# Performance work log

Hardware: AMD Instinct MI355X
Metric: run time of the kernel (lower is better)

The kernel has to match this reference:

```python
import jax, jax.numpy as jnp
import numpy as np

M_HIST = 5        # Anderson history depth (m=5 in anderson_solver)
N_POWER = 20      # power iterations to estimate sigma for spectral_norm
REG = 1e-4        # Tikhonov regularization on the Anderson LS system
MAX_ITER = 25     # deq_max_iter


def _l2norm(x):
    return x / (jnp.linalg.norm(x) + 1e-12)


def spectral_normalize(W):
    # torch spectral_norm: W / sigma, sigma = u^T W v with u,v from power iteration
    u = _l2norm(jnp.ones((W.shape[0],), W.dtype))
    def body(_, u):
        v = _l2norm(W.T @ u)
        return _l2norm(W @ v)
    u = jax.lax.fori_loop(0, N_POWER, body, u)
    v = _l2norm(W.T @ u)
    u = jax.lax.stop_gradient(u)
    v = jax.lax.stop_gradient(v)
    sigma = u @ (W @ v)
    return W / sigma


def make_f(W1, b1, W2, b2):
    W1s = spectral_normalize(W1)
    W2s = spectral_normalize(W2)
    def f(z, context):
        h = jnp.tanh(jnp.concatenate([z, context], axis=-1) @ W1s.T + b1)
        return jnp.tanh(h @ W2s.T + b2)
    return f


def anderson(f, x0, context, max_iter, m=M_HIST):
    # Mirrors anderson_solver, including its duplicated warm-up step.
    X = [x0]
    F = [f(x0, context)]
    x = F[0]; X.append(x); F.append(f(x, context))
    x = F[0]; X.append(x); F.append(f(x, context))
    for _k in range(2, max_iter):
        m_k = min(len(X) - 1, m)
        dX = jnp.stack([X[-i] - X[-i - 1] for i in range(1, m_k + 1)], axis=-1)  # [B,d,mk]
        dF = jnp.stack([F[-i] - F[-i - 1] for i in range(1, m_k + 1)], axis=-1)
        dG = dF - dX
        A = jnp.einsum('bdi,bdj->bij', dG, dG) + REG * jnp.eye(m_k, dtype=x0.dtype)
        r = F[-1] - X[-1]
        Bv = jnp.einsum('bdi,bd->bi', dG, r)
        alpha = jnp.linalg.solve(A, Bv[..., None])[..., 0]          # [B,mk]
        x = F[-1] - jnp.einsum('bdi,bi->bd', dF, alpha)
        X.append(x)
        F.append(f(x, context))
        if len(X) > m + 1:
            X.pop(0); F.pop(0)
    return X[-1]


def setup_inputs() -> dict:
    key = jax.random.key(0)
    ks = jax.random.split(key, 5)
    B, X_DIM, LATENT, HIDDEN = 2048, 256, 256, 1024
    context = jax.random.normal(ks[0], (B, X_DIM), jnp.float32)
    W1 = jax.random.normal(ks[1], (HIDDEN, LATENT + X_DIM), jnp.float32) / np.sqrt(LATENT + X_DIM)
    b1 = jax.random.normal(ks[2], (HIDDEN,), jnp.float32) * 0.01
    W2 = jax.random.normal(ks[3], (LATENT, HIDDEN), jnp.float32) / np.sqrt(HIDDEN)
    b2 = jax.random.normal(ks[4], (LATENT,), jnp.float32) * 0.01
    return {"context": context, "W1": W1, "b1": b1, "W2": W2, "b2": b2}


def reference(context, W1, b1, W2, b2):
    f = make_f(W1, b1, W2, b2)
    z0 = jnp.zeros((context.shape[0], W2.shape[0]), context.dtype)
    z_star = anderson(f, z0, context, MAX_ITER)
    return z_star
```

## Files before the change

kernel.cpp:

```cpp
#include <hip/hip_runtime.h>
#include <hip/hip_bf16.h>


#define B_ROWS 2048
#define D_LAT  256
#define D_CTX  256
#define D_HID  1024
#define KCAT   512
#define SLOT   (B_ROWS * D_LAT)
#define NRING  7

typedef __bf16 bf16x8 __attribute__((ext_vector_type(8)));
typedef float f32x4 __attribute__((ext_vector_type(4)));
typedef unsigned short u16;

__global__ void init_kernel(const float* __restrict__ ctx,
                            __hip_bfloat16* __restrict__ zc,
                            float* __restrict__ vA, float* __restrict__ uA,
                            float* __restrict__ G1p, float* __restrict__ G2) {
  int i = blockIdx.x * 256 + threadIdx.x;
  if (i < B_ROWS * KCAT) {
    int b = i >> 9, c = i & 511;
    float v = (c < 256) ? 0.0f : ctx[b * 256 + (c - 256)];
    zc[i] = __float2bfloat16(v);
  }
  if (i < 512 * 512) G1p[i] = 0.0f;
  if (i < 256 * 256) G2[i] = 0.0f;
  if (i < KCAT) vA[i] = 0.0f;
  if (i < D_LAT) uA[i] = 1.0f;
}

__global__ __launch_bounds__(256) void gram_kernel(
    const float* __restrict__ W1, const float* __restrict__ W2,
    float* __restrict__ G1p, float* __restrict__ G2) {
  __shared__ float As[32][66];
  __shared__ float Bs[32][34];
  const int tid = threadIdx.x;
  const int tx = tid & 15, ty = tid >> 4;

  const float* X; float* G; int N, ti, tj, k0base; bool modeA;
  int b = blockIdx.x;
  if (b < 1024) {
    modeA = true; X = W1; G = G1p; N = 512;
    int s = b >> 7, t = b & 127;
    ti = t >> 4; tj = t & 15; k0base = s * 128;
  } else {
    modeA = false; b -= 1024; X = W2; G = G2; N = 256;
    int s = b >> 5, t = b & 31;
    ti = t >> 3; tj = t & 7; k0base = s * 128;
  }

  float acc[4][2] = {};
  for (int k0 = k0base; k0 < k0base + 128; k0 += 32) {
    if (modeA) {
      for (int idx = tid; idx < 2048; idx += 256) {
        int r = idx & 63, c = idx >> 6;
        As[c][r] = X[(size_t)(k0 + c) * 512 + ti * 64 + r];
      }
      for (int idx = tid; idx < 1024; idx += 256) {
        int r = idx & 31, c = idx >> 5;
        Bs[c][r] = X[(size_t)(k0 + c) * 512 + tj * 32 + r];
      }
    } else {
      for (int idx = tid; idx < 2048; idx += 256) {
        int c = idx & 31, r = idx >> 5;
        As[c][r] = X[(size_t)(ti * 64 + r) * 1024 + k0 + c];
      }
      for (int idx = tid; idx < 1024; idx += 256) {
        int c = idx & 31, r = idx >> 5;
        Bs[c][r] = X[(size_t)(tj * 32 + r) * 1024 + k0 + c];
      }
    }
    __syncthreads();
#pragma unroll
    for (int kk = 0; kk < 32; kk++) {
      const float2* ap = (const float2*)&As[kk][ty * 4];
      float2 a0 = ap[0], a1 = ap[1];
      float2 b0 = *(const float2*)&Bs[kk][tx * 2];
      float a[4] = {a0.x, a0.y, a1.x, a1.y};
      float bb[2] = {b0.x, b0.y};
#pragma unroll
      for (int i = 0; i < 4; i++)
#pragma unroll
        for (int j = 0; j < 2; j++) acc[i][j] += a[i] * bb[j];
    }
    __syncthreads();
  }
#pragma unroll
  for (int i = 0; i < 4; i++)
#pragma unroll
    for (int j = 0; j < 2; j++)
      atomicAdd(&G[(size_t)(ti * 64 + ty * 4 + i) * N + tj * 32 + tx * 2 + j],
                acc[i][j]);
}

__global__ __launch_bounds__(256) void colsum_kernel(
    const float* __restrict__ W1, float* __restrict__ vA) {
  int b = blockIdx.x;
  for (int c = threadIdx.x; c < KCAT; c += 256) {
    float s = 0.f;
#pragma unroll
    for (int r = 0; r < 16; r++) s += W1[(size_t)(16 * b + r) * KCAT + c];
    atomicAdd(&vA[c], s);
  }
}

__global__ __launch_bounds__(256) void pmv_kernel(
    const float* __restrict__ G1p, const float* __restrict__ G2,
    const float* __restrict__ vi, float* __restrict__ vo,
    const float* __restrict__ ui, float* __restrict__ uo, int g1_active) {
  int gw = blockIdx.x * 4 + (threadIdx.x >> 6);
  int lane = threadIdx.x & 63;
  const float* G; const float* in; float* out; int n, r;
  if (gw < 512) {
    if (!g1_active) return;
    G = G1p; in = vi; out = vo; n = 512; r = gw;
  } else {
    G = G2; in = ui; out = uo; n = 256; r = gw - 512;
  }
  const float4* Gr = (const float4*)(G + (size_t)r * n);
  const float4* uv = (const float4*)in;
  float acc = 0.f;
  for (int c = lane; c < (n >> 2); c += 64) {
    float4 g = Gr[c], u = uv[c];
    acc += g.x * u.x + g.y * u.y + g.z * u.z + g.w * u.w;
  }
  for (int off = 32; off; off >>= 1) acc += __shfl_down(acc, off, 64);
  if (lane == 0) out[r] = 0.25f * acc;
}

__global__ __launch_bounds__(256) void sigma_kernel(
    const float* __restrict__ vA, const float* __restrict__ vB,
    const float* __restrict__ uA, const float* __restrict__ uB,
    float* __restrict__ sig) {
  float s[4] = {0.f, 0.f, 0.f, 0.f};
  for (int i = threadIdx.x; i < KCAT; i += 256) {
    s[0] += vA[i] * vB[i];
    s[1] += vA[i] * vA[i];
  }
  for (int i = threadIdx.x; i < D_LAT; i += 256) {
    s[2] += uA[i] * uA[i];
    s[3] += uA[i] * uB[i];
  }
  __shared__ float red[4][4];
  int lane = threadIdx.x & 63, w = threadIdx.x >> 6;
  for (int k = 0; k < 4; k++) {
    float a = s[k];
    for (int off = 32; off; off >>= 1) a += __shfl_down(a, off, 64);
    if (lane == 0) red[k][w] = a;
  }
  __syncthreads();
  if (threadIdx.x == 0) {
    float d0 = red[0][0] + red[0][1] + red[0][2] + red[0][3];
    float d1 = red[1][0] + red[1][1] + red[1][2] + red[1][3];
    float d2 = red[2][0] + red[2][1] + red[2][2] + red[2][3];
    float d3 = red[3][0] + red[3][1] + red[3][2] + red[3][3];
    sig[0] = sqrtf(0.25f * d0 / d1);
    sig[1] = sqrtf(0.25f * d2 / d3);
  }
}

__global__ void wfold_kernel(const float* __restrict__ W1,
                             const float* __restrict__ W2,
                             const float* __restrict__ sig,
                             __hip_bfloat16* __restrict__ W1b,
                             __hip_bfloat16* __restrict__ W2b) {
  int i = blockIdx.x * 256 + threadIdx.x;
  if (i < D_HID * KCAT) W1b[i] = __float2bfloat16(W1[i] * sig[0]);
  int j = i - D_HID * KCAT;
  if (j >= 0 && j < D_LAT * D_HID) W2b[j] = __float2bfloat16(W2[j] * sig[1]);
}

__global__ void warm1_kernel(const float* __restrict__ Fh,
                             float* __restrict__ Xh,
                             __hip_bfloat16* __restrict__ zc) {
  int i = blockIdx.x * 256 + threadIdx.x;
  float v = Fh[i];
  Xh[SLOT + i] = v;
  zc[(i >> 8) * KCAT + (i & 255)] = __float2bfloat16(v);
}
__global__ void warm2_kernel(const float* __restrict__ Fh,
                             float* __restrict__ Xh, float* __restrict__ Fw) {
  int i = blockIdx.x * 256 + threadIdx.x;
  Xh[2 * SLOT + i] = Fh[i];
  Fw[2 * SLOT + i] = Fh[SLOT + i];
}

template <int BM, int BN, bool OUT_BF16>
__global__ __launch_bounds__(256) void gemm_mfma(
    const __hip_bfloat16* __restrict__ A, const __hip_bfloat16* __restrict__ W,
    int K, const float* __restrict__ bias, float* __restrict__ Cf,
    __hip_bfloat16* __restrict__ Cb, int N) {
  __shared__ __align__(16) u16 lds[(BM + BN) * 64];
  u16* As = lds;
  u16* Ws = lds + BM * 64;
  const int tid = threadIdx.x;
  const int lane = tid & 63;
  const int wid = tid >> 6;
  const int wy = wid >> 1, wx = wid & 1;
  constexpr int WM = BM / 2, WN = BN / 2;
  constexpr int MB = WM / 16, NB = WN / 16;
  const int bm = blockIdx.x * BM;
  const int bn = blockIdx.y * BN;
  const int rlo = lane & 15, quad = lane >> 4;

  f32x4 acc[MB][NB] = {};

  for (int k0 = 0; k0 < K; k0 += 64) {
    for (int c = tid; c < BM * 8; c += 256) {
      int r = c >> 3, o = (c & 7) ^ (r & 7);
      __builtin_amdgcn_global_load_lds(
          (const __attribute__((address_space(1))) void*)(A + (size_t)(bm + r) * K + k0 + o * 8),
          (__attribute__((address_space(3))) void*)(As + c * 8), 16, 0, 0);
    }
    for (int c = tid; c < BN * 8; c += 256) {
      int r = c >> 3, o = (c & 7) ^ (r & 7);
      __builtin_amdgcn_global_load_lds(
          (const __attribute__((address_space(1))) void*)(W + (size_t)(bn + r) * K + k0 + o * 8),
          (__attribute__((address_space(3))) void*)(Ws + c * 8), 16, 0, 0);
    }
    __syncthreads();
#pragma unroll
    for (int kk = 0; kk < 2; kk++) {
      bf16x8 af[MB], bfr[NB];
#pragma unroll
      for (int mb = 0; mb < MB; mb++) {
        int r = wy * WM + mb * 16 + rlo;
        int o = (kk * 4 + quad) ^ (r & 7);
        af[mb] = *(const bf16x8*)(As + (r * 8 + o) * 8);
      }
#pragma unroll
      for (int nb = 0; nb < NB; nb++) {
        int r = wx * WN + nb * 16 + rlo;
        int o = (kk * 4 + quad) ^ (r & 7);
        bfr[nb] = *(const bf16x8*)(Ws + (r * 8 + o) * 8);
      }
#pragma unroll
      for (int mb = 0; mb < MB; mb++)
#pragma unroll
        for (int nb = 0; nb < NB; nb++)
          acc[mb][nb] = __builtin_amdgcn_mfma_f32_16x16x32_bf16(
              af[mb], bfr[nb], acc[mb][nb], 0, 0, 0);
    }
    __syncthreads();
  }

#pragma unroll
  for (int mb = 0; mb < MB; mb++) {
#pragma unroll
    for (int nb = 0; nb < NB; nb++) {
      int n = bn + wx * WN + nb * 16 + rlo;
      float bv = bias[n];
#pragma unroll
      for (int rg = 0; rg < 4; rg++) {
        int m = bm + wy * WM + mb * 16 + quad * 4 + rg;
        float val = tanhf(acc[mb][nb][rg] + bv);
        if constexpr (OUT_BF16) {
          Cb[(size_t)m * N + n] = __float2bfloat16(val);
        } else {
          Cf[(size_t)m * N + n] = val;
        }
      }
    }
  }
}

template <int MK>
__global__ __launch_bounds__(256) void anderson_step_kernel(
    const float* __restrict__ Xh, const float* __restrict__ Fh,
    float* __restrict__ Xw, __hip_bfloat16* __restrict__ zc, int t) {
  const int lane = threadIdx.x & 63;
  const int wid = threadIdx.x >> 6;
  const int b = blockIdx.x * 4 + wid;
  const int base = b * D_LAT + 4 * lane;

  f32x4 f[MK + 1], x[MK + 1];
#pragma unroll
  for (int i = 0; i <= MK; i++) {
    int sl = (t - 1 - i) % NRING;
    f[i] = *(const f32x4*)(Fh + (size_t)sl * SLOT + base);
    x[i] = *(const f32x4*)(Xh + (size_t)sl * SLOT + base);
  }

  const f32x4 r = f[0] - x[0];
  f32x4 dF[MK], dG[MK];
#pragma unroll
  for (int i = 0; i < MK; i++) {
    dF[i] = f[i] - f[i + 1];
    dG[i] = dF[i] - (x[i] - x[i + 1]);
  }

  constexpr int NV = MK * (MK + 1) / 2 + MK;
  float vals[NV];
  {
    int p = 0;
#pragma unroll
    for (int i = 0; i < MK; i++)
#pragma unroll
      for (int j = i; j < MK; j++) {
        f32x4 q = dG[i] * dG[j];
        vals[p++] = q[0] + q[1] + q[2] + q[3];
      }
#pragma unroll
    for (int i = 0; i < MK; i++) {
      f32x4 q = dG[i] * r;
      vals[p++] = q[0] + q[1] + q[2] + q[3];
    }
  }
#pragma unroll
  for (int off = 1; off <= 32; off <<= 1)
#pragma unroll
    for (int v = 0; v < NV; v++) vals[v] += __shfl_xor(vals[v], off, 64);

  float A[MK][MK], bv[MK], alpha[MK];
  {
    int p = 0;
#pragma unroll
    for (int i = 0; i < MK; i++)
#pragma unroll
      for (int j = i; j < MK; j++) {
        A[i][j] = vals[p];
        A[j][i] = vals[p];
        p++;
      }
#pragma unroll
    for (int i = 0; i < MK; i++) A[i][i] += 1e-4f;
#pragma unroll
    for (int i = 0; i < MK; i++) bv[i] = vals[p++];
  }

#pragma unroll
  for (int c = 0; c < MK; c++) {
    float inv = 1.0f / A[c][c];
#pragma unroll
    for (int rr = c + 1; rr < MK; rr++) {
      float fct = A[rr][c] * inv;
#pragma unroll
      for (int cc = c; cc < MK; cc++) A[rr][cc] -= fct * A[c][cc];
      bv[rr] -= fct * bv[c];
    }
  }
#pragma unroll
  for (int i = MK - 1; i >= 0; i--) {
    float s = bv[i];
#pragma unroll
    for (int j = i + 1; j < MK; j++) s -= A[i][j] * alpha[j];
    alpha[i] = s / A[i][i];
  }

  f32x4 xo = f[0];
#pragma unroll
  for (int i = 0; i < MK; i++) xo -= dF[i] * alpha[i];
  *(f32x4*)(Xw + base) = xo;
  if (zc != nullptr) {
    union { __hip_bfloat16 h[4]; unsigned long long u; } cv;
#pragma unroll
    for (int j = 0; j < 4; j++) cv.h[j] = __float2bfloat16(xo[j]);
    *(unsigned long long*)(zc + (size_t)b * KCAT + 4 * lane) = cv.u;
  }
}

static void eval_f(const __hip_bfloat16* zc, const __hip_bfloat16* W1b,
                   const __hip_bfloat16* W2b, const float* b1, const float* b2,
                   __hip_bfloat16* hb, float* Fout, hipStream_t stream) {
  gemm_mfma<64, 64, true><<<dim3(B_ROWS / 64, D_HID / 64), 256, 0, stream>>>(
      zc, W1b, KCAT, b1, nullptr, hb, D_HID);
  gemm_mfma<32, 32, false><<<dim3(B_ROWS / 32, D_LAT / 32), 256, 0, stream>>>(
      hb, W2b, D_HID, b2, Fout, nullptr, D_LAT);
}

extern "C" void kernel_launch(void* const* d_in, const int* in_sizes, int n_in,
                              void* d_out, int out_size, void* d_ws,
                              size_t ws_size, hipStream_t stream) {
  const float* ctx = (const float*)d_in[0];
  const float* W1 = (const float*)d_in[1];
  const float* b1 = (const float*)d_in[2];
  const float* W2 = (const float*)d_in[3];
  const float* b2 = (const float*)d_in[4];
  float* out = (float*)d_out;

  float* ws = (float*)d_ws;
  float* sig = ws;
  float* vA = ws + 16;
  float* vB = vA + KCAT;
  float* uA = vB + KCAT;
  float* uB = uA + D_LAT;
  float* G1p = uB + D_LAT;
  float* G2 = G1p + KCAT * KCAT;
  float* Xh = G2 + D_LAT * D_LAT;
  float* Fh = Xh + NRING * SLOT;
  __hip_bfloat16* W1b = (__hip_bfloat16*)(Fh + NRING * SLOT);
  __hip_bfloat16* W2b = W1b + D_HID * KCAT;
  __hip_bfloat16* zc = W2b + D_LAT * D_HID;
  __hip_bfloat16* hb = zc + B_ROWS * KCAT;

  init_kernel<<<(B_ROWS * KCAT + 255) / 256, 256, 0, stream>>>(ctx, zc, vA, uA,
                                                               G1p, G2);
  gram_kernel<<<1280, 256, 0, stream>>>(W1, W2, G1p, G2);
  colsum_kernel<<<64, 256, 0, stream>>>(W1, vA);

  for (int it = 1; it <= 21; it++) {
    const float* vi; float* vo;
    const float* ui; float* uo;
    if (it & 1) { vi = vB; vo = vA; ui = uA; uo = uB; }
    else        { vi = vA; vo = vB; ui = uB; uo = uA; }
    pmv_kernel<<<192, 256, 0, stream>>>(G1p, G2, vi, vo, ui, uo, it >= 2);
  }
  sigma_kernel<<<1, 256, 0, stream>>>(vA, vB, uA, uB, sig);
  wfold_kernel<<<(D_HID * KCAT + D_LAT * D_HID + 255) / 256, 256, 0, stream>>>(
      W1, W2, sig, W1b, W2b);

  hipMemsetAsync(Xh, 0, SLOT * sizeof(float), stream);

  eval_f(zc, W1b, W2b, b1, b2, hb, Fh, stream);
  warm1_kernel<<<SLOT / 256, 256, 0, stream>>>(Fh, Xh, zc);
  eval_f(zc, W1b, W2b, b1, b2, hb, Fh + SLOT, stream);
  warm2_kernel<<<SLOT / 256, 256, 0, stream>>>(Fh, Xh, Fh);

  for (int t = 3; t <= 25; t++) {
    int mk = (t - 1 < 5) ? (t - 1) : 5;
    float* Xw = (t == 25) ? out : (Xh + (t % NRING) * SLOT);
    __hip_bfloat16* zarg = (t == 25) ? nullptr : zc;
    dim3 g(B_ROWS / 4);
    if (mk == 2)
      anderson_step_kernel<2><<<g, 256, 0, stream>>>(Xh, Fh, Xw, zarg, t);
    else if (mk == 3)
      anderson_step_kernel<3><<<g, 256, 0, stream>>>(Xh, Fh, Xw, zarg, t);
    else if (mk == 4)
      anderson_step_kernel<4><<<g, 256, 0, stream>>>(Xh, Fh, Xw, zarg, t);
    else
      anderson_step_kernel<5><<<g, 256, 0, stream>>>(Xh, Fh, Xw, zarg, t);
    if (t < 25) {
      eval_f(zc, W1b, W2b, b1, b2, hb, Fh + (t % NRING) * SLOT, stream);
    }
  }
}
```

Before: 820.1 us.

## Square Gram matrices to halve power iterations and double-buffer GEMM LDS

Adds a kernel that computes the square of each Gram matrix, so the power iteration runs as about half as many matrix-vector launches using G^2 plus a couple of plain G steps. Separately, the MFMA GEMM now uses two LDS buffers and issues the next k-tile's global-to-LDS loads before computing the current one, with K made a compile-time constant. This targets the serial chain of tiny launches and the load/compute stall in the hot GEMMs. The trade-offs are an extra 512x512 fp32 matmul, more fp32 rounding in the squared matrices, and doubled LDS per block, which could reduce occupancy.

```diff
diff --git a/kernel.cpp b/kernel.cpp
--- a/kernel.cpp
+++ b/kernel.cpp
@@ -105,28 +105,73 @@
   }
 }
 
+__global__ __launch_bounds__(256) void gsq_kernel(
+    const float* __restrict__ G1p, const float* __restrict__ G2,
+    float* __restrict__ H1, float* __restrict__ H2) {
+  __shared__ float As[32][66];
+  __shared__ float Bs[32][34];
+  const int tid = threadIdx.x;
+  const int tx = tid & 15, ty = tid >> 4;
+  const float* X; float* H; int N, ti, tj;
+  int b = blockIdx.x;
+  if (b < 128) { X = G1p; H = H1; N = 512; ti = b >> 4; tj = b & 15; }
+  else { b -= 128; X = G2; H = H2; N = 256; ti = b >> 3; tj = b & 7; }
+
+  float acc[4][2] = {};
+  for (int k0 = 0; k0 < N; k0 += 32) {
+    for (int idx = tid; idx < 2048; idx += 256) {
+      int c = idx & 31, r = idx >> 5;
+      As[c][r] = X[(size_t)(ti * 64 + r) * N + k0 + c];
+    }
+    for (int idx = tid; idx < 1024; idx += 256) {
+      int c = idx & 31, r = idx >> 5;
+      Bs[c][r] = X[(size_t)(tj * 32 + r) * N + k0 + c];
+    }
+    __syncthreads();
+#pragma unroll
+    for (int kk = 0; kk < 32; kk++) {
+      const float2* ap = (const float2*)&As[kk][ty * 4];
+      float2 a0 = ap[0], a1 = ap[1];
+      float2 b0 = *(const float2*)&Bs[kk][tx * 2];
+      float a[4] = {a0.x, a0.y, a1.x, a1.y};
+      float bb[2] = {b0.x, b0.y};
+#pragma unroll
+      for (int i = 0; i < 4; i++)
+#pragma unroll
+        for (int j = 0; j < 2; j++) acc[i][j] += a[i] * bb[j];
+    }
+    __syncthreads();
+  }
+#pragma unroll
+  for (int i = 0; i < 4; i++)
+#pragma unroll
+    for (int j = 0; j < 2; j++)
+      H[(size_t)(ti * 64 + ty * 4 + i) * N + tj * 32 + tx * 2 + j] = acc[i][j];
+}
+
 __global__ __launch_bounds__(256) void pmv_kernel(
-    const float* __restrict__ G1p, const float* __restrict__ G2,
+    const float* __restrict__ Mv, const float* __restrict__ Mu,
     const float* __restrict__ vi, float* __restrict__ vo,
-    const float* __restrict__ ui, float* __restrict__ uo, int g1_active) {
+    const float* __restrict__ ui, float* __restrict__ uo,
+    float scale, int v_active) {
   int gw = blockIdx.x * 4 + (threadIdx.x >> 6);
   int lane = threadIdx.x & 63;
-  const float* G; const float* in; float* out; int n, r;
+  const float* M; const float* in; float* out; int n, r;
   if (gw < 512) {
-    if (!g1_active) return;
-    G = G1p; in = vi; out = vo; n = 512; r = gw;
+    if (!v_active) return;
+    M = Mv; in = vi; out = vo; n = 512; r = gw;
   } else {
-    G = G2; in = ui; out = uo; n = 256; r = gw - 512;
-  }
-  const float4* Gr = (const float4*)(G + (size_t)r * n);
+    M = Mu; in = ui; out = uo; n = 256; r = gw - 512;
+  }
+  const float4* Mr = (const float4*)(M + (size_t)r * n);
   const float4* uv = (const float4*)in;
   float acc = 0.f;
   for (int c = lane; c < (n >> 2); c += 64) {
-    float4 g = Gr[c], u = uv[c];
+    float4 g = Mr[c], u = uv[c];
     acc += g.x * u.x + g.y * u.y + g.z * u.z + g.w * u.w;
   }
   for (int off = 32; off; off >>= 1) acc += __shfl_down(acc, off, 64);
-  if (lane == 0) out[r] = 0.25f * acc;
+  if (lane == 0) out[r] = scale * acc;
 }
 
 __global__ __launch_bounds__(256) void sigma_kernel(
@@ -186,27 +231,28 @@
   Fw[2 * SLOT + i] = Fh[SLOT + i];
 }
 
-template <int BM, int BN, bool OUT_BF16>
+template <int BM, int BN, int K, bool OUT_BF16>
 __global__ __launch_bounds__(256) void gemm_mfma(
     const __hip_bfloat16* __restrict__ A, const __hip_bfloat16* __restrict__ W,
-    int K, const float* __restrict__ bias, float* __restrict__ Cf,
+    const float* __restrict__ bias, float* __restrict__ Cf,
     __hip_bfloat16* __restrict__ Cb, int N) {
-  __shared__ __align__(16) u16 lds[(BM + BN) * 64];
-  u16* As = lds;
-  u16* Ws = lds + BM * 64;
+  __shared__ __align__(16) u16 lds[2][(BM + BN) * 64];
   const int tid = threadIdx.x;
   const int lane = tid & 63;
   const int wid = tid >> 6;
   const int wy = wid >> 1, wx = wid & 1;
   constexpr int WM = BM / 2, WN = BN / 2;
   constexpr int MB = WM / 16, NB = WN / 16;
+  constexpr int NK = K / 64;
   const int bm = blockIdx.x * BM;
   const int bn = blockIdx.y * BN;
   const int rlo = lane & 15, quad = lane >> 4;
 
   f32x4 acc[MB][NB] = {};
 
-  for (int k0 = 0; k0 < K; k0 += 64) {
+  auto stage = [&](u16* base, int k0) {
+    u16* As = base;
+    u16* Ws = base + BM * 64;
     for (int c = tid; c < BM * 8; c += 256) {
       int r = c >> 3, o = (c & 7) ^ (r & 7);
       __builtin_amdgcn_global_load_lds(
@@ -219,7 +265,10 @@
           (const __attribute__((address_space(1))) void*)(W + (size_t)(bn + r) * K + k0 + o * 8),
           (__attribute__((address_space(3))) void*)(Ws + c * 8), 16, 0, 0);
     }
-    __syncthreads();
+  };
+  auto compute = [&](const u16* base) {
+    const u16* As = base;
+    const u16* Ws = base + BM * 64;
 #pragma unroll
     for (int kk = 0; kk < 2; kk++) {
       bf16x8 af[MB], bfr[NB];
@@ -242,7 +291,17 @@
           acc[mb][nb] = __builtin_amdgcn_mfma_f32_16x16x32_bf16(
               af[mb], bfr[nb], acc[mb][nb], 0, 0, 0);
     }
-    __syncthreads();
+  };
+
+  stage(&lds[0][0], 0);
+  __syncthreads();
+#pragma unroll 2
+  for (int step = 0; step < NK; step++) {
+    u16* cur = (step & 1) ? &lds[1][0] : &lds[0][0];
+    u16* nxt = (step & 1) ? &lds[0][0] : &lds[1][0];
+    if (step + 1 < NK) stage(nxt, (step + 1) * 64);
+    compute(cur);
+    if (step + 1 < NK) __syncthreads();
   }
 
 #pragma unroll
@@ -363,10 +422,11 @@
 static void eval_f(const __hip_bfloat16* zc, const __hip_bfloat16* W1b,
                    const __hip_bfloat16* W2b, const float* b1, const float* b2,
                    __hip_bfloat16* hb, float* Fout, hipStream_t stream) {
-  gemm_mfma<64, 64, true><<<dim3(B_ROWS / 64, D_HID / 64), 256, 0, stream>>>(
-      zc, W1b, KCAT, b1, nullptr, hb, D_HID);
-  gemm_mfma<32, 32, false><<<dim3(B_ROWS / 32, D_LAT / 32), 256, 0, stream>>>(
-      hb, W2b, D_HID, b2, Fout, nullptr, D_LAT);
+  gemm_mfma<64, 64, KCAT, true><<<dim3(B_ROWS / 64, D_HID / 64), 256, 0,
+                                  stream>>>(zc, W1b, b1, nullptr, hb, D_HID);
+  gemm_mfma<32, 32, D_HID, false><<<dim3(B_ROWS / 32, D_LAT / 32), 256, 0,
+                                    stream>>>(hb, W2b, b2, Fout, nullptr,
+                                              D_LAT);
 }
 
 extern "C" void kernel_launch(void* const* d_in, const int* in_sizes, int n_in,
@@ -387,7 +447,9 @@
   float* uB = uA + D_LAT;
   float* G1p = uB + D_LAT;
   float* G2 = G1p + KCAT * KCAT;
-  float* Xh = G2 + D_LAT * D_LAT;
+  float* H1 = G2 + D_LAT * D_LAT;
+  float* H2 = H1 + KCAT * KCAT;
+  float* Xh = H2 + D_LAT * D_LAT;
   float* Fh = Xh + NRING * SLOT;
   __hip_bfloat16* W1b = (__hip_bfloat16*)(Fh + NRING * SLOT);
   __hip_bfloat16* W2b = W1b + D_HID * KCAT;
@@ -398,15 +460,18 @@
                                                                G1p, G2);
   gram_kernel<<<1280, 256, 0, stream>>>(W1, W2, G1p, G2);
   colsum_kernel<<<64, 256, 0, stream>>>(W1, vA);
-
-  for (int it = 1; it <= 21; it++) {
-    const float* vi; float* vo;
-    const float* ui; float* uo;
-    if (it & 1) { vi = vB; vo = vA; ui = uA; uo = uB; }
-    else        { vi = vA; vo = vB; ui = uB; uo = uA; }
-    pmv_kernel<<<192, 256, 0, stream>>>(G1p, G2, vi, vo, ui, uo, it >= 2);
-  }
-  sigma_kernel<<<1, 256, 0, stream>>>(vA, vB, uA, uB, sig);
+  gsq_kernel<<<160, 256, 0, stream>>>(G1p, G2, H1, H2);
+
+  pmv_kernel<<<192, 256, 0, stream>>>(G1p, G2, vA, vB, uA, uB, 0.25f, 0);
+  for (int j = 0; j < 9; j++) {
+    const float *vi_, *ui_; float *vo_, *uo_;
+    if ((j & 1) == 0) { vi_ = vA; vo_ = vB; ui_ = uB; uo_ = uA; }
+    else              { vi_ = vB; vo_ = vA; ui_ = uA; uo_ = uB; }
+    pmv_kernel<<<192, 256, 0, stream>>>(H1, H2, vi_, vo_, ui_, uo_, 0.0625f, 1);
+  }
+  pmv_kernel<<<192, 256, 0, stream>>>(G1p, G2, vB, vA, uA, uB, 0.25f, 1);
+  pmv_kernel<<<192, 256, 0, stream>>>(G1p, G2, vA, vB, uB, uA, 0.25f, 1);
+  sigma_kernel<<<1, 256, 0, stream>>>(vB, vA, uB, uA, sig);
   wfold_kernel<<<(D_HID * KCAT + D_LAT * D_HID + 255) / 256, 256, 0, stream>>>(
       W1, W2, sig, W1b, W2b);
 
```

Result: no change. 815.1 us (-0.6%).
